# Kernel optimization log

Hardware: AMD Instinct MI355X
Metric: run time of the kernel (lower is better)

The kernel has to match this reference:

```python
import jax, jax.numpy as jnp
import numpy as np

N = 1_000_000
D_IN = 128
D_OUT = 128
S = 65_536


def setup_inputs() -> dict:
    key = jax.random.key(0)
    k1, k2, k3, k4 = jax.random.split(key, 4)
    element_embeddings = jax.random.normal(k1, (N, D_IN), dtype=jnp.float32)
    element_to_sample_map = jnp.sort(
        jax.random.randint(k2, (N,), 0, S, dtype=jnp.int64)
    )
    # nn.Linear(D_IN, 1, bias=False) weight -> vector [D_IN]
    w_att = jax.random.normal(k3, (D_IN,), dtype=jnp.float32) * (1.0 / np.sqrt(D_IN))
    # nn.Linear(D_IN, D_OUT, bias=False) weight [D_OUT, D_IN]
    w_out = jax.random.normal(k4, (D_OUT, D_IN), dtype=jnp.float32) * (1.0 / np.sqrt(D_IN))
    return {
        "element_embeddings": element_embeddings,
        "element_to_sample_map": element_to_sample_map,
        "num_samples": S,
        "w_att": w_att,
        "w_out": w_out,
    }


def reference(element_embeddings, element_to_sample_map, num_samples, w_att, w_out):
    seg = element_to_sample_map
    # attention scores [N]
    scores = element_embeddings @ w_att
    # segment log-softmax (numerically stable, single max/sum pass)
    seg_max = jax.ops.segment_max(scores, seg, num_segments=num_samples)
    shifted = scores - seg_max[seg]
    exp_shifted = jnp.exp(shifted)
    seg_sum = jax.ops.segment_sum(exp_shifted, seg, num_segments=num_samples)
    log_probs = shifted - jnp.log(seg_sum)[seg]
    attention_probs = jnp.exp(log_probs)  # [N]
    # output projection then weighted scatter-sum per segment -> [S, D_OUT]
    projected = element_embeddings @ w_out.T
    return jax.ops.segment_sum(
        projected * attention_probs[:, None], seg, num_segments=num_samples
    )
```

## Files before the change

kernel.cpp:

```cpp
#include <hip/hip_runtime.h>
#include <hip/hip_bf16.h>

#define N_ELEM 1000000
#define D 128
#define S_SEG 65536
#define SEGW 8
#define NBLK 2048
#define NEG_BIG (-1e30f)

__global__ __launch_bounds__(256) void k_bounds(const int* __restrict__ seg,
                                                int* __restrict__ off) {
    int s = blockIdx.x * blockDim.x + threadIdx.x;
    if (s > S_SEG) return;
    int lo = 0, hi = N_ELEM;
    while (lo < hi) {
        int mid = (lo + hi) >> 1;
        if (seg[mid] < s) lo = mid + 1; else hi = mid;
    }
    off[s] = lo;
}

__device__ __forceinline__ float halfReduce(float d) {
    #pragma unroll
    for (int off = 1; off <= 16; off <<= 1)
        d += __shfl_xor(d, off, 64);
    return d;
}

__device__ __forceinline__ float dot4(float4 v, float4 w) {
    return fmaf(v.x, w.x, fmaf(v.y, w.y, fmaf(v.z, w.z, v.w * w.w)));
}

__device__ __forceinline__ void osm_step(float& m, float& l, float4& a,
                                         float d, float4 v, bool valid) {
    float mn = valid ? fmaxf(m, d) : m;
    float scale = __expf(m - mn);
    float p = valid ? __expf(d - mn) : 0.f;
    m = mn;
    l = fmaf(l, scale, p);
    a.x = fmaf(a.x, scale, p * v.x);
    a.y = fmaf(a.y, scale, p * v.y);
    a.z = fmaf(a.z, scale, p * v.z);
    a.w = fmaf(a.w, scale, p * v.w);
}

__device__ __forceinline__ void osm_merge(float& m1, float& l1, float4& a1,
                                          float m2, float l2, float4 a2) {
    float m = fmaxf(m1, m2);
    float s1 = __expf(m1 - m), s2 = __expf(m2 - m);
    l1 = l1 * s1 + l2 * s2;
    a1.x = a1.x * s1 + a2.x * s2;
    a1.y = a1.y * s1 + a2.y * s2;
    a1.z = a1.z * s1 + a2.z * s2;
    a1.w = a1.w * s1 + a2.w * s2;
    m1 = m;
}

__global__ __launch_bounds__(256) void k_fused(
        const float* __restrict__ emb, const int* __restrict__ off,
        const float* __restrict__ watt, float* __restrict__ out) {
    const int lane = threadIdx.x & 63;
    const int half = lane >> 5;
    const int hl   = lane & 31;
    const int wid  = blockIdx.x * 4 + (threadIdx.x >> 6);
    const float4 wv = reinterpret_cast<const float4*>(watt)[hl];
    const float4* emb4 = reinterpret_cast<const float4*>(emb);
    float4* out4 = reinterpret_cast<float4*>(out);

    const int s0 = wid * SEGW;
    int offv[SEGW + 1];
    #pragma unroll
    for (int i = 0; i <= SEGW; ++i) offv[i] = off[s0 + i];

    #pragma unroll 1
    for (int si = 0; si < SEGW; ++si) {
        const int beg = offv[si], end = offv[si + 1];
        float  mA = NEG_BIG, lA = 0.f; float4 aA = {0.f, 0.f, 0.f, 0.f};
        float  mB = NEG_BIG, lB = 0.f; float4 aB = {0.f, 0.f, 0.f, 0.f};
        for (int e = beg; e < end; e += 8) {
            int ra = min(e     + half, N_ELEM - 1);
            int rb = min(e + 2 + half, N_ELEM - 1);
            int rc = min(e + 4 + half, N_ELEM - 1);
            int rd = min(e + 6 + half, N_ELEM - 1);
            float4 v0 = emb4[(size_t)ra * 32 + hl];
            float4 v1 = emb4[(size_t)rb * 32 + hl];
            float4 v2 = emb4[(size_t)rc * 32 + hl];
            float4 v3 = emb4[(size_t)rd * 32 + hl];
            float d0 = halfReduce(dot4(v0, wv));
            float d1 = halfReduce(dot4(v1, wv));
            float d2 = halfReduce(dot4(v2, wv));
            float d3 = halfReduce(dot4(v3, wv));
            osm_step(mA, lA, aA, d0, v0, e     + half < end);
            osm_step(mB, lB, aB, d1, v1, e + 2 + half < end);
            osm_step(mA, lA, aA, d2, v2, e + 4 + half < end);
            osm_step(mB, lB, aB, d3, v3, e + 6 + half < end);
        }
        osm_merge(mA, lA, aA, mB, lB, aB);
        float  mo = __shfl_xor(mA, 32, 64);
        float  lo = __shfl_xor(lA, 32, 64);
        float4 ao;
        ao.x = __shfl_xor(aA.x, 32, 64);
        ao.y = __shfl_xor(aA.y, 32, 64);
        ao.z = __shfl_xor(aA.z, 32, 64);
        ao.w = __shfl_xor(aA.w, 32, 64);
        osm_merge(mA, lA, aA, mo, lo, ao);
        float inv = (lA > 0.f) ? 1.0f / lA : 0.f;
        if (half == 0) {
            float4 r = {aA.x * inv, aA.y * inv, aA.z * inv, aA.w * inv};
            out4[(size_t)(s0 + si) * 32 + hl] = r;
        }
    }
}

#define PAD 132
__global__ __launch_bounds__(256) void k_proj(
        float* __restrict__ out, const float* __restrict__ wout) {
    __shared__ float As[128 * PAD];
    __shared__ float Bs[128 * PAD];
    const int tid = threadIdx.x;
    const int r0 = blockIdx.x * 128;
    for (int idx = tid; idx < 128 * 128; idx += 256) {
        int a = idx >> 7, k = idx & 127;
        As[k * PAD + a] = out[(size_t)(r0 + a) * D + k];
        Bs[k * PAD + a] = wout[(size_t)a * D + k];
    }
    __syncthreads();
    const int tx = tid & 15, ty = tid >> 4;
    const int rr = ty * 8, cc = tx * 8;
    float acc[8][8] = {};
    for (int k = 0; k < 128; ++k) {
        float a[8], b[8];
        *reinterpret_cast<float4*>(&a[0]) = *reinterpret_cast<const float4*>(&As[k * PAD + rr]);
        *reinterpret_cast<float4*>(&a[4]) = *reinterpret_cast<const float4*>(&As[k * PAD + rr + 4]);
        *reinterpret_cast<float4*>(&b[0]) = *reinterpret_cast<const float4*>(&Bs[k * PAD + cc]);
        *reinterpret_cast<float4*>(&b[4]) = *reinterpret_cast<const float4*>(&Bs[k * PAD + cc + 4]);
        #pragma unroll
        for (int i = 0; i < 8; ++i)
            #pragma unroll
            for (int j = 0; j < 8; ++j)
                acc[i][j] = fmaf(a[i], b[j], acc[i][j]);
    }
    #pragma unroll
    for (int i = 0; i < 8; ++i) {
        float4 o0 = {acc[i][0], acc[i][1], acc[i][2], acc[i][3]};
        float4 o1 = {acc[i][4], acc[i][5], acc[i][6], acc[i][7]};
        *reinterpret_cast<float4*>(&out[(size_t)(r0 + rr + i) * D + cc])     = o0;
        *reinterpret_cast<float4*>(&out[(size_t)(r0 + rr + i) * D + cc + 4]) = o1;
    }
}

extern "C" void kernel_launch(void* const* d_in, const int* in_sizes, int n_in,
                              void* d_out, int out_size, void* d_ws, size_t ws_size,
                              hipStream_t stream) {
    const float* emb  = (const float*)d_in[0];
    const int*   seg  = (const int*)d_in[1];
    const float* watt = (const float*)d_in[3];
    const float* wout = (const float*)d_in[4];
    float* out = (float*)d_out;

    int* off = (int*)d_ws;

    k_bounds<<<(S_SEG + 256) / 256, 256, 0, stream>>>(seg, off);
    k_fused <<<NBLK, 256, 0, stream>>>(emb, off, watt, out);
    k_proj  <<<S_SEG / 128, 256, 0, stream>>>(out, wout);
}
```

Before: 183.5 us.

## Fuse segment-boundary search into main kernel and software-pipeline row loads

Removes the separate binary-search kernel. Each wave now computes its own 9 segment offsets on lanes 0..8 and broadcasts them with shuffles, which saves one launch and the workspace round trip. The inner loop changes from a 4-load batch per iteration to a 2-row prefetch double buffer with a step of 4 elements. This lowers memory-level parallelism per iteration but overlaps each load with the previous compute. The binary search now sits at the start of every wave and serializes up to 20 dependent global loads before streaming begins.

New measurement: 179.2 us. 2.3% less time.

```diff
diff --git a/kernel.cpp b/kernel.cpp
--- a/kernel.cpp
+++ b/kernel.cpp
@@ -7,18 +7,6 @@
 #define SEGW 8
 #define NBLK 2048
 #define NEG_BIG (-1e30f)
-
-__global__ __launch_bounds__(256) void k_bounds(const int* __restrict__ seg,
-                                                int* __restrict__ off) {
-    int s = blockIdx.x * blockDim.x + threadIdx.x;
-    if (s > S_SEG) return;
-    int lo = 0, hi = N_ELEM;
-    while (lo < hi) {
-        int mid = (lo + hi) >> 1;
-        if (seg[mid] < s) lo = mid + 1; else hi = mid;
-    }
-    off[s] = lo;
-}
 
 __device__ __forceinline__ float halfReduce(float d) {
     #pragma unroll
@@ -57,7 +45,7 @@
 }
 
 __global__ __launch_bounds__(256) void k_fused(
-        const float* __restrict__ emb, const int* __restrict__ off,
+        const float* __restrict__ emb, const int* __restrict__ seg,
         const float* __restrict__ watt, float* __restrict__ out) {
     const int lane = threadIdx.x & 63;
     const int half = lane >> 5;
@@ -68,42 +56,45 @@
     float4* out4 = reinterpret_cast<float4*>(out);
 
     const int s0 = wid * SEGW;
-    int offv[SEGW + 1];
-    #pragma unroll
-    for (int i = 0; i <= SEGW; ++i) offv[i] = off[s0 + i];
+    int lo = 0;
+    if (lane <= SEGW) {
+        const int target = s0 + lane;
+        int hi = N_ELEM;
+        while (lo < hi) {
+            int mid = (lo + hi) >> 1;
+            if (seg[mid] < target) lo = mid + 1; else hi = mid;
+        }
+    }
 
     #pragma unroll 1
     for (int si = 0; si < SEGW; ++si) {
-        const int beg = offv[si], end = offv[si + 1];
+        const int beg = __shfl(lo, si, 64);
+        const int end = __shfl(lo, si + 1, 64);
         float  mA = NEG_BIG, lA = 0.f; float4 aA = {0.f, 0.f, 0.f, 0.f};
         float  mB = NEG_BIG, lB = 0.f; float4 aB = {0.f, 0.f, 0.f, 0.f};
-        for (int e = beg; e < end; e += 8) {
-            int ra = min(e     + half, N_ELEM - 1);
-            int rb = min(e + 2 + half, N_ELEM - 1);
-            int rc = min(e + 4 + half, N_ELEM - 1);
-            int rd = min(e + 6 + half, N_ELEM - 1);
-            float4 v0 = emb4[(size_t)ra * 32 + hl];
-            float4 v1 = emb4[(size_t)rb * 32 + hl];
-            float4 v2 = emb4[(size_t)rc * 32 + hl];
-            float4 v3 = emb4[(size_t)rd * 32 + hl];
-            float d0 = halfReduce(dot4(v0, wv));
-            float d1 = halfReduce(dot4(v1, wv));
-            float d2 = halfReduce(dot4(v2, wv));
-            float d3 = halfReduce(dot4(v3, wv));
-            osm_step(mA, lA, aA, d0, v0, e     + half < end);
-            osm_step(mB, lB, aB, d1, v1, e + 2 + half < end);
-            osm_step(mA, lA, aA, d2, v2, e + 4 + half < end);
-            osm_step(mB, lB, aB, d3, v3, e + 6 + half < end);
+        if (beg < end) {
+            float4 c0 = emb4[(size_t)min(beg + half,     N_ELEM - 1) * 32 + hl];
+            float4 c1 = emb4[(size_t)min(beg + 2 + half, N_ELEM - 1) * 32 + hl];
+            #pragma unroll 1
+            for (int e = beg; e < end; e += 4) {
+                float4 n0 = emb4[(size_t)min(e + 4 + half, N_ELEM - 1) * 32 + hl];
+                float4 n1 = emb4[(size_t)min(e + 6 + half, N_ELEM - 1) * 32 + hl];
+                float d0 = halfReduce(dot4(c0, wv));
+                float d1 = halfReduce(dot4(c1, wv));
+                osm_step(mA, lA, aA, d0, c0, (e + half)     < end);
+                osm_step(mB, lB, aB, d1, c1, (e + 2 + half) < end);
+                c0 = n0; c1 = n1;
+            }
         }
         osm_merge(mA, lA, aA, mB, lB, aB);
         float  mo = __shfl_xor(mA, 32, 64);
-        float  lo = __shfl_xor(lA, 32, 64);
+        float  lo2 = __shfl_xor(lA, 32, 64);
         float4 ao;
         ao.x = __shfl_xor(aA.x, 32, 64);
         ao.y = __shfl_xor(aA.y, 32, 64);
         ao.z = __shfl_xor(aA.z, 32, 64);
         ao.w = __shfl_xor(aA.w, 32, 64);
-        osm_merge(mA, lA, aA, mo, lo, ao);
+        osm_merge(mA, lA, aA, mo, lo2, ao);
         float inv = (lA > 0.f) ? 1.0f / lA : 0.f;
         if (half == 0) {
             float4 r = {aA.x * inv, aA.y * inv, aA.z * inv, aA.w * inv};
@@ -158,9 +149,6 @@
     const float* wout = (const float*)d_in[4];
     float* out = (float*)d_out;
 
-    int* off = (int*)d_ws;
-
-    k_bounds<<<(S_SEG + 256) / 256, 256, 0, stream>>>(seg, off);
-    k_fused <<<NBLK, 256, 0, stream>>>(emb, off, watt, out);
-    k_proj  <<<S_SEG / 128, 256, 0, stream>>>(out, wout);
+    k_fused<<<NBLK, 256, 0, stream>>>(emb, seg, watt, out);
+    k_proj <<<S_SEG / 128, 256, 0, stream>>>(out, wout);
 }
```
